# Optimization experiments

Measured on AMD Instinct MI355X. Metric: run time of the kernel, lower is better.

Reference implementation:

```python
import jax, jax.numpy as jnp
import numpy as np

# dims: d_model D, d_inner DI=2*D, d_state S, dt_rank R, conv kernel K, layers NL
D, DI, S, R, K, NL = 512, 1024, 16, 32, 4, 6
B, L = 4, 1024
EPS = 1e-5


def _ln(x, w, b):
    m = x.mean(-1, keepdims=True)
    v = ((x - m) ** 2).mean(-1, keepdims=True)
    return (x - m) * jax.lax.rsqrt(v + EPS) * w + b


def _causal_conv(x, w, b):
    # depthwise causal conv1d: x [B,L,DI], w [DI,K], left-pad K-1 (matches Conv1d(padding=K-1) then crop)
    xp = jnp.pad(x, ((0, 0), (K - 1, 0), (0, 0)))
    y = sum(xp[:, k:k + x.shape[1], :] * w[:, k] for k in range(K))
    return y + b


def _mamba(h, in_w, cw, cb, xp_w, dt_w, dt_b, A_log, Dp, out_w):
    # h: [B,L,D]
    xz = jnp.einsum('bld,ed->ble', h, in_w)        # [B,L,2*DI]
    x, z = jnp.split(xz, 2, axis=-1)
    x = jax.nn.silu(_causal_conv(x, cw, cb))       # [B,L,DI]
    dbc = jnp.einsum('bld,ed->ble', x, xp_w)       # [B,L,R+2S]
    dt_r, Bm, Cm = dbc[..., :R], dbc[..., R:R + S], dbc[..., R + S:]
    dt = jax.nn.softplus(jnp.einsum('blr,dr->bld', dt_r, dt_w) + dt_b)  # [B,L,DI]
    A = -jnp.exp(A_log)                            # [DI,S]

    def step(hst, inp):
        dt_t, B_t, C_t, x_t = inp                  # [B,DI],[B,S],[B,S],[B,DI]
        dA = jnp.exp(dt_t[..., None] * A)          # [B,DI,S]
        hst = dA * hst + (dt_t * x_t)[..., None] * B_t[:, None, :]
        y = jnp.einsum('bds,bs->bd', hst, C_t)
        return hst, y

    h0 = jnp.zeros((x.shape[0], DI, S), x.dtype)
    xs = (dt.transpose(1, 0, 2), Bm.transpose(1, 0, 2), Cm.transpose(1, 0, 2), x.transpose(1, 0, 2))
    _, ys = jax.lax.scan(step, h0, xs)
    y = ys.transpose(1, 0, 2) + x * Dp
    y = y * jax.nn.silu(z)
    return jnp.einsum('bld,ed->ble', y, out_w)     # [B,L,D]


def setup_inputs() -> dict:
    key = jax.random.key(0)
    ks = jax.random.split(key, 10)
    n = lambda k, shp, s: s * jax.random.normal(k, shp, jnp.float32)
    inp = {}
    inp['xs_pad'] = jax.random.normal(ks[0], (B, L, D), jnp.float32)
    inp['ilens'] = jax.random.randint(ks[1], (B,), 1, L + 1)
    inp['norm_w'] = jnp.ones((NL, D), jnp.float32)
    inp['norm_b'] = jnp.zeros((NL, D), jnp.float32)
    inp['in_proj_w'] = n(ks[2], (NL, 2 * DI, D), 0.02)
    inp['conv_w'] = n(ks[3], (NL, DI, K), 0.1)
    inp['conv_b'] = jnp.zeros((NL, DI), jnp.float32)
    inp['x_proj_w'] = n(ks[4], (NL, R + 2 * S, DI), 0.02)
    inp['dt_proj_w'] = n(ks[5], (NL, DI, R), 0.1)
    inp['dt_proj_b'] = n(ks[6], (NL, DI), 0.01)
    inp['A_log'] = jnp.log(jnp.broadcast_to(jnp.arange(1, S + 1, dtype=jnp.float32), (NL, DI, S)))
    inp['D_param'] = jnp.ones((NL, DI), jnp.float32)
    inp['out_proj_w'] = n(ks[7], (NL, D, DI), 0.02)
    inp['normf_w'] = jnp.ones((D,), jnp.float32)
    inp['normf_b'] = jnp.zeros((D,), jnp.float32)
    inp['after_w'] = jnp.ones((D,), jnp.float32)
    inp['after_b'] = jnp.zeros((D,), jnp.float32)
    return inp


def reference(xs_pad, ilens, norm_w, norm_b, in_proj_w, conv_w, conv_b, x_proj_w,
              dt_proj_w, dt_proj_b, A_log, D_param, out_proj_w,
              normf_w, normf_b, after_w, after_b):
    hidden = xs_pad
    residual = None
    for i in range(NL):
        residual = hidden + residual if residual is not None else hidden
        hn = _ln(residual, norm_w[i], norm_b[i])
        hidden = _mamba(hn, in_proj_w[i], conv_w[i], conv_b[i], x_proj_w[i],
                        dt_proj_w[i], dt_proj_b[i], A_log[i], D_param[i], out_proj_w[i])
    residual = hidden + residual
    out = _ln(residual, normf_w, normf_b)   # norm_f
    out = _ln(out, after_w, after_b)        # after_norm (normalize_before=True)
    olens = jnp.minimum(ilens, L)
    return out, olens
```

## Files before the change

### kernel.cpp

```cpp
#include <hip/hip_runtime.h>
#include <hip/hip_bf16.h>
#include <math.h>

#define D_   512
#define DI_  1024
#define S_   16
#define R_   32
#define KC_  4
#define NL_  6
#define B_   4
#define L_   1024
#define BL_  (B_*L_)
#define NC_  64
#define CL_  (L_/NC_)
#define BDI_ (B_*DI_)
#define LOG2E 1.44269504f
#define SKX  8
#define SKO  4

typedef __hip_bfloat16 bf16;
typedef __attribute__((ext_vector_type(8))) short bf16x8;
typedef __attribute__((ext_vector_type(4))) float f32x4;
typedef unsigned short u16;

#define QIDX(s, c, bd) (((size_t)(s) * NC_ + (c)) * BDI_ + (bd))

__device__ __forceinline__ float b2f(u16 u) {
  union { unsigned int i; float f; } x; x.i = ((unsigned int)u) << 16; return x.f;
}

__device__ __forceinline__ float softplus_f(float v) {
  float e = __expf(-fabsf(v));
  return fmaxf(v, 0.f) + __logf(1.f + e);
}

__device__ __forceinline__ void gload16(const void* g, void* l) {
  __builtin_amdgcn_global_load_lds((const __attribute__((address_space(1))) void*)g,
                                   (__attribute__((address_space(3))) void*)l, 16, 0, 0);
}

#define N1_ (NL_*2*DI_*D_)
#define N2_ (N1_ + NL_*D_*DI_)
#define N3_ (N2_ + NL_*128*DI_)
__global__ void setup_k(const float* __restrict__ in_w, const float* __restrict__ out_w,
                        const float* __restrict__ xp_w,
                        bf16* __restrict__ inw_b, bf16* __restrict__ outw_b,
                        bf16* __restrict__ xpw_b) {
  for (int i = blockIdx.x * blockDim.x + threadIdx.x; i < N3_; i += gridDim.x * blockDim.x) {
    if (i < N1_) {
      inw_b[i] = __float2bfloat16(in_w[i]);
    } else if (i < N2_) {
      int j = i - N1_;
      outw_b[j] = __float2bfloat16(out_w[j]);
    } else {
      int j = i - N2_;
      int c = j & (DI_ - 1);
      int r = (j >> 10) & 127;
      int l = j >> 17;
      float v = (r < 64) ? xp_w[((size_t)l * 64 + r) * DI_ + c] : 0.f;
      xpw_b[j] = __float2bfloat16(v);
    }
  }
}

__global__ __launch_bounds__(128) void addln_k(
    const float* __restrict__ x0, const u16* __restrict__ parts,
    float* __restrict__ resid, const float* __restrict__ w, const float* __restrict__ b,
    bf16* __restrict__ hn, int first)
{
  __shared__ float red[4];
  const int row = blockIdx.x, t = threadIdx.x;
  const int lane = t & 63, wv = t >> 6;
  float4 v;
  if (first) {
    v = *(const float4*)(x0 + (size_t)row * D_ + t * 4);
  } else {
    const size_t ps = (size_t)BL_ * D_;
    const size_t o = (size_t)row * D_ + t * 4;
    v.x = 0.f; v.y = 0.f; v.z = 0.f; v.w = 0.f;
    #pragma unroll
    for (int p = 0; p < SKO; ++p) {
      ushort4 q = *(const ushort4*)(parts + p * ps + o);
      v.x += b2f(q.x); v.y += b2f(q.y); v.z += b2f(q.z); v.w += b2f(q.w);
    }
    float4 r = *(const float4*)(resid + o);
    v.x += r.x; v.y += r.y; v.z += r.z; v.w += r.w;
  }
  *(float4*)(resid + (size_t)row * D_ + t * 4) = v;
  float s = v.x + v.y + v.z + v.w;
  float ss = v.x*v.x + v.y*v.y + v.z*v.z + v.w*v.w;
  #pragma unroll
  for (int o = 32; o > 0; o >>= 1) { s += __shfl_xor(s, o); ss += __shfl_xor(ss, o); }
  if (lane == 0) { red[wv * 2] = s; red[wv * 2 + 1] = ss; }
  __syncthreads();
  float S = red[0] + red[2], SS = red[1] + red[3];
  float m = S * (1.f / D_), var = SS * (1.f / D_) - m * m;
  float rs = rsqrtf(var + 1e-5f);
  float4 w4 = *(const float4*)(w + t * 4);
  float4 b4 = *(const float4*)(b + t * 4);
  bf16* o = hn + (size_t)row * D_ + t * 4;
  o[0] = __float2bfloat16((v.x - m) * rs * w4.x + b4.x);
  o[1] = __float2bfloat16((v.y - m) * rs * w4.y + b4.y);
  o[2] = __float2bfloat16((v.z - m) * rs * w4.z + b4.z);
  o[3] = __float2bfloat16((v.w - m) * rs * w4.w + b4.w);
}

__global__ __launch_bounds__(256) void gemm_bt(
    const bf16* __restrict__ A, int lda,
    const bf16* __restrict__ B, int ldb,
    bf16* __restrict__ Cb,
    int K, int Nact, int M, int epi)
{
  __shared__ __align__(16) bf16 As[128 * 32];
  __shared__ __align__(16) bf16 Bs[128 * 32];
  const int tid = threadIdx.x;
  const int wave = tid >> 6, lane = tid & 63;
  const int bm = blockIdx.x * 128, bn = blockIdx.y * 128;
  const int kz = blockIdx.z;
  const int Kc = K / gridDim.z;
  const int k0 = kz * Kc, k1 = k0 + Kc;
  const int wr = (wave >> 1) << 6, wc = (wave & 1) << 6;
  const int srow = lane >> 2, scg = lane & 3;
  const int rA = lane & 15, kq = (lane >> 4) << 3;
  f32x4 acc[4][4] = {};
  for (int kt = k0; kt < k1; kt += 32) {
    __syncthreads();
    #pragma unroll
    for (int p = 0; p < 2; ++p) {
      int chunk = wave * 2 + p;
      int row = (chunk << 4) + srow;
      gload16(A + (size_t)(bm + row) * lda + kt + scg * 8, &As[chunk * 512]);
      gload16(B + (size_t)(bn + row) * ldb + kt + scg * 8, &Bs[chunk * 512]);
    }
    __syncthreads();
    bf16x8 af[4], bq[4];
    #pragma unroll
    for (int m = 0; m < 4; ++m) af[m] = *(const bf16x8*)&As[(wr + m * 16 + rA) * 32 + kq];
    #pragma unroll
    for (int n = 0; n < 4; ++n) bq[n] = *(const bf16x8*)&Bs[(wc + n * 16 + rA) * 32 + kq];
    #pragma unroll
    for (int m = 0; m < 4; ++m)
      #pragma unroll
      for (int n = 0; n < 4; ++n)
        acc[m][n] = __builtin_amdgcn_mfma_f32_16x16x32_bf16(af[m], bq[n], acc[m][n], 0, 0, 0);
  }
  const int cr = (lane >> 4) << 2, cc = lane & 15;
  const size_t pbase = (epi == 1) ? (size_t)kz * M * Nact : 0;
  #pragma unroll
  for (int m = 0; m < 4; ++m)
    #pragma unroll
    for (int n = 0; n < 4; ++n) {
      int col = bn + wc + n * 16 + cc;
      if (col >= Nact) continue;
      #pragma unroll
      for (int j = 0; j < 4; ++j) {
        size_t row = (size_t)(bm + wr + m * 16 + cr + j);
        Cb[pbase + row * Nact + col] = __float2bfloat16(acc[m][n][j]);
      }
    }
}

__global__ __launch_bounds__(256) void redx_k(
    const u16* __restrict__ part, float* __restrict__ dbc)
{
  int i = blockIdx.x * 256 + threadIdx.x;
  const size_t ps = (size_t)BL_ * 64;
  float v = 0.f;
  #pragma unroll
  for (int p = 0; p < SKX; ++p) v += b2f(part[p * ps + i]);
  dbc[i] = v;
}

__global__ __launch_bounds__(256) void conv_silu_k(
    const u16* __restrict__ xz, const float* __restrict__ cw, const float* __restrict__ cb,
    bf16* __restrict__ xcb)
{
  int g = blockIdx.x * 256 + threadIdx.x;
  int dq = g & (DI_ / 8 - 1);
  int bl = g >> 7;
  int l = bl & (L_ - 1), b = bl >> 10;
  int d = dq * 8;
  float a[8], wv[8][KC_];
  #pragma unroll
  for (int e = 0; e < 8; ++e) {
    float4 w4 = *(const float4*)(cw + (d + e) * KC_);
    wv[e][0] = w4.x; wv[e][1] = w4.y; wv[e][2] = w4.z; wv[e][3] = w4.w;
    a[e] = cb[d + e];
  }
  #pragma unroll
  for (int k = 0; k < KC_; ++k) {
    int lt = l + k - 3;
    if (lt < 0) continue;
    bf16x8 xv = *(const bf16x8*)(xz + (size_t)(b * L_ + lt) * (2 * DI_) + d);
    #pragma unroll
    for (int e = 0; e < 8; ++e) a[e] += b2f((u16)xv[e]) * wv[e][k];
  }
  bf16 o8[8];
  #pragma unroll
  for (int e = 0; e < 8; ++e) {
    float v = a[e] / (1.f + __expf(-a[e]));
    o8[e] = __float2bfloat16(v);
  }
  *(bf16x8*)(xcb + (size_t)bl * DI_ + d) = *(const bf16x8*)o8;
}


__global__ __launch_bounds__(256) void scanA_k(
    const u16* __restrict__ x, const float* __restrict__ dbc,
    const float* __restrict__ dtw, const float* __restrict__ dtbias,
    const float* __restrict__ A_log, float* __restrict__ sumdt,
    bf16* __restrict__ q, bf16* __restrict__ dtb)
{
  __shared__ float BS[CL_ * 16];
  __shared__ float DTR[CL_ * 32];
  const int tid = threadIdx.x;
  int g = blockIdx.x * 256 + tid;
  int d = g & (DI_ - 1);
  int cb = g >> 10;
  int b = cb & (B_ - 1);
  int c = cb >> 2;
  {
    int step = tid >> 4, off = tid & 15;
    BS[tid] = dbc[((size_t)(b * L_ + c * CL_ + step)) * 64 + R_ + off];
    int f = tid * 2;
    int st2 = f >> 5, of2 = f & 31;
    float2 v = *(const float2*)(dbc + ((size_t)(b * L_ + c * CL_ + st2)) * 64 + of2);
    DTR[f] = v.x; DTR[f + 1] = v.y;
  }
  float wv[R_];
  #pragma unroll
  for (int r = 0; r < R_; r += 4) {
    float4 w4 = *(const float4*)(dtw + (size_t)d * R_ + r);
    wv[r] = w4.x; wv[r + 1] = w4.y; wv[r + 2] = w4.z; wv[r + 3] = w4.w;
  }
  const float bias = dtbias[d];
  const float An2b = -expf(A_log[(size_t)d * S_]) * LOG2E;
  bool fast = true;
  #pragma unroll
  for (int s = 1; s < S_; ++s) {
    float a = -expf(A_log[(size_t)d * S_ + s]) * LOG2E;
    fast = fast && (fabsf(a - (float)(s + 1) * An2b) <= 1e-5f * fabsf(a));
  }
  __syncthreads();
  float h[S_] = {};
  float sdt = 0.f;
  const size_t base = ((size_t)b * L_ + c * CL_) * DI_ + d;
  float cx = b2f(x[base]);
  float dtv;
  {
    float v = bias;
    #pragma unroll
    for (int r = 0; r < R_; r += 4) {
      float4 dv = *(const float4*)&DTR[r];
      v += dv.x * wv[r] + dv.y * wv[r + 1] + dv.z * wv[r + 2] + dv.w * wv[r + 3];
    }
    dtv = softplus_f(v);
  }
  for (int i = 0; i < CL_; ++i) {
    const int ip = (i + 1 < CL_) ? i + 1 : i;
    float nx = b2f(x[base + (size_t)ip * DI_]);
    float vn = bias;
    #pragma unroll
    for (int r = 0; r < R_; r += 4) {
      float4 dv = *(const float4*)&DTR[ip * 32 + r];
      vn += dv.x * wv[r] + dv.y * wv[r + 1] + dv.z * wv[r + 2] + dv.w * wv[r + 3];
    }
    dtb[base + (size_t)i * DI_] = __float2bfloat16(dtv);
    sdt += dtv;
    float u = dtv * cx;
    float Bv[S_];
    *(float4*)&Bv[0]  = *(const float4*)&BS[i * 16 + 0];
    *(float4*)&Bv[4]  = *(const float4*)&BS[i * 16 + 4];
    *(float4*)&Bv[8]  = *(const float4*)&BS[i * 16 + 8];
    *(float4*)&Bv[12] = *(const float4*)&BS[i * 16 + 12];
    float da[S_];
    if (fast) {
      float E1 = exp2f(dtv * An2b);
      float E2 = E1 * E1;
      float E4 = E2 * E2;
      da[0] = E1; da[1] = E2; da[2] = E2 * E1; da[3] = E4;
      #pragma unroll
      for (int s = 4; s < S_; ++s) da[s] = da[s - 4] * E4;
    } else {
      #pragma unroll
      for (int s = 0; s < S_; ++s)
        da[s] = exp2f(dtv * (-expf(A_log[(size_t)d * S_ + s]) * LOG2E));
    }
    #pragma unroll
    for (int s = 0; s < S_; ++s) h[s] = da[s] * h[s] + u * Bv[s];
    dtv = softplus_f(vn);
    cx = nx;
  }
  int bd = b * DI_ + d;
  sumdt[(size_t)c * BDI_ + bd] = sdt;
  #pragma unroll
  for (int s = 0; s < S_; ++s) q[QIDX(s, c, bd)] = __float2bfloat16(h[s]);
}

__global__ __launch_bounds__(256) void scanB_k(
    const float* __restrict__ sumdt, const u16* __restrict__ q,
    const float* __restrict__ A_log, bf16* __restrict__ hi)
{
  int g = blockIdx.x * 256 + threadIdx.x;
  int s = g >> 12;
  int bd = g & (BDI_ - 1);
  int d = bd & (DI_ - 1);
  float An2 = -expf(A_log[(size_t)d * S_ + s]) * LOG2E;
  float h = 0.f;
  float sd = sumdt[bd];
  float qq = b2f(q[(size_t)s * NC_ * BDI_ + bd]);
  for (int c = 0; c < NC_; ++c) {
    float sdn = sd, qn = qq;
    if (c + 1 < NC_) {
      sdn = sumdt[(size_t)(c + 1) * BDI_ + bd];
      qn  = b2f(q[QIDX(s, c + 1, bd)]);
    }
    hi[QIDX(s, c, bd)] = __float2bfloat16(h);
    h = exp2f(An2 * sd) * h + qq;
    sd = sdn; qq = qn;
  }
}

__global__ __launch_bounds__(256) void scanC_k(
    const u16* __restrict__ dt, const u16* __restrict__ x, const float* __restrict__ dbc,
    const float* __restrict__ A_log, const float* __restrict__ Dp, const u16* __restrict__ xz,
    const u16* __restrict__ hi, bf16* __restrict__ y)
{
  __shared__ float BCS[CL_ * 32];
  const int tid = threadIdx.x;
  int g = blockIdx.x * 256 + tid;
  int d = g & (DI_ - 1);
  int cb = g >> 10;
  int b = cb & (B_ - 1);
  int c = cb >> 2;
  {
    int f = tid * 2;
    int step = f >> 5, off = f & 31;
    float2 v = *(const float2*)(dbc + ((size_t)(b * L_ + c * CL_ + step)) * 64 + R_ + off);
    BCS[f] = v.x; BCS[f + 1] = v.y;
  }
  const float An2b = -expf(A_log[(size_t)d * S_]) * LOG2E;
  bool fast = true;
  #pragma unroll
  for (int s = 1; s < S_; ++s) {
    float a = -expf(A_log[(size_t)d * S_ + s]) * LOG2E;
    fast = fast && (fabsf(a - (float)(s + 1) * An2b) <= 1e-5f * fabsf(a));
  }
  int bd = b * DI_ + d;
  float h[S_];
  #pragma unroll
  for (int s = 0; s < S_; ++s) h[s] = b2f(hi[QIDX(s, c, bd)]);
  __syncthreads();
  float dpv = Dp[d];
  const size_t rid0 = (size_t)b * L_ + c * CL_;
  const size_t base = rid0 * DI_ + d;
  float cdt = b2f(dt[base]), cx = b2f(x[base]);
  float cz = b2f(xz[rid0 * (2 * DI_) + DI_ + d]);
  float Ecur = exp2f(cdt * An2b);
  for (int i = 0; i < CL_; ++i) {
    const int ip = (i + 1 < CL_) ? i + 1 : i;
    float ndt = b2f(dt[base + (size_t)ip * DI_]);
    float nx  = b2f(x[base + (size_t)ip * DI_]);
    float nz  = b2f(xz[(rid0 + ip) * (2 * DI_) + DI_ + d]);
    float Enext = exp2f(ndt * An2b);
    float u = cdt * cx;
    float Bv[S_], Cv[S_];
    *(float4*)&Bv[0]  = *(const float4*)&BCS[i * 32 + 0];
    *(float4*)&Bv[4]  = *(const float4*)&BCS[i * 32 + 4];
    *(float4*)&Bv[8]  = *(const float4*)&BCS[i * 32 + 8];
    *(float4*)&Bv[12] = *(const float4*)&BCS[i * 32 + 12];
    *(float4*)&Cv[0]  = *(const float4*)&BCS[i * 32 + 16];
    *(float4*)&Cv[4]  = *(const float4*)&BCS[i * 32 + 20];
    *(float4*)&Cv[8]  = *(const float4*)&BCS[i * 32 + 24];
    *(float4*)&Cv[12] = *(const float4*)&BCS[i * 32 + 28];
    float da[S_];
    if (fast) {
      float E1 = Ecur;
      float E2 = E1 * E1;
      float E4 = E2 * E2;
      da[0] = E1; da[1] = E2; da[2] = E2 * E1; da[3] = E4;
      #pragma unroll
      for (int s = 4; s < S_; ++s) da[s] = da[s - 4] * E4;
    } else {
      #pragma unroll
      for (int s = 0; s < S_; ++s)
        da[s] = exp2f(cdt * (-expf(A_log[(size_t)d * S_ + s]) * LOG2E));
    }
    float acc = 0.f;
    #pragma unroll
    for (int s = 0; s < S_; ++s) {
      h[s] = da[s] * h[s] + u * Bv[s];
      acc += h[s] * Cv[s];
    }
    acc += cx * dpv;
    acc *= cz / (1.f + __expf(-cz));
    y[(rid0 + i) * DI_ + d] = __float2bfloat16(acc);
    cdt = ndt; cx = nx; cz = nz; Ecur = Enext;
  }
}

__global__ __launch_bounds__(128) void final_k(
    const u16* __restrict__ parts, const float* __restrict__ res,
    const float* __restrict__ fw, const float* __restrict__ fb,
    const float* __restrict__ aw, const float* __restrict__ ab,
    const int* __restrict__ ilens, float* __restrict__ out, int outN)
{
  __shared__ float red[4];
  const int row = blockIdx.x, t = threadIdx.x;
  const int lane = t & 63, wv = t >> 6;
  const size_t ps = (size_t)BL_ * D_;
  const size_t o0 = (size_t)row * D_ + t * 4;
  float4 v; v.x = 0.f; v.y = 0.f; v.z = 0.f; v.w = 0.f;
  #pragma unroll
  for (int p = 0; p < SKO; ++p) {
    ushort4 q = *(const ushort4*)(parts + p * ps + o0);
    v.x += b2f(q.x); v.y += b2f(q.y); v.z += b2f(q.z); v.w += b2f(q.w);
  }
  float4 r = *(const float4*)(res + o0);
  v.x += r.x; v.y += r.y; v.z += r.z; v.w += r.w;
  float s = v.x + v.y + v.z + v.w;
  float ss = v.x*v.x + v.y*v.y + v.z*v.z + v.w*v.w;
  #pragma unroll
  for (int o = 32; o > 0; o >>= 1) { s += __shfl_xor(s, o); ss += __shfl_xor(ss, o); }
  if (lane == 0) { red[wv * 2] = s; red[wv * 2 + 1] = ss; }
  __syncthreads();
  float S = red[0] + red[2], SS = red[1] + red[3];
  float m = S * (1.f / D_), var = SS * (1.f / D_) - m * m;
  float rs = rsqrtf(var + 1e-5f);
  float4 w4 = *(const float4*)(fw + t * 4);
  float4 b4 = *(const float4*)(fb + t * 4);
  float4 x1;
  x1.x = (v.x - m) * rs * w4.x + b4.x;
  x1.y = (v.y - m) * rs * w4.y + b4.y;
  x1.z = (v.z - m) * rs * w4.z + b4.z;
  x1.w = (v.w - m) * rs * w4.w + b4.w;
  __syncthreads();
  float s2 = x1.x + x1.y + x1.z + x1.w;
  float ss2 = x1.x*x1.x + x1.y*x1.y + x1.z*x1.z + x1.w*x1.w;
  #pragma unroll
  for (int o = 32; o > 0; o >>= 1) { s2 += __shfl_xor(s2, o); ss2 += __shfl_xor(ss2, o); }
  if (lane == 0) { red[wv * 2] = s2; red[wv * 2 + 1] = ss2; }
  __syncthreads();
  float S2 = red[0] + red[2], SS2 = red[1] + red[3];
  float m2 = S2 * (1.f / D_), var2 = SS2 * (1.f / D_) - m2 * m2;
  float rs2 = rsqrtf(var2 + 1e-5f);
  float4 aw4 = *(const float4*)(aw + t * 4);
  float4 ab4 = *(const float4*)(ab + t * 4);
  float4 o;
  o.x = (x1.x - m2) * rs2 * aw4.x + ab4.x;
  o.y = (x1.y - m2) * rs2 * aw4.y + ab4.y;
  o.z = (x1.z - m2) * rs2 * aw4.z + ab4.z;
  o.w = (x1.w - m2) * rs2 * aw4.w + ab4.w;
  *(float4*)(out + (size_t)row * D_ + t * 4) = o;
  if (row == 0 && t < B_) {
    int q = ilens[t];
    out[outN + t] = (float)(q < L_ ? q : L_);
  }
}

extern "C" void kernel_launch(void* const* d_in, const int* in_sizes, int n_in,
                              void* d_out, int out_size, void* d_ws, size_t ws_size,
                              hipStream_t stream) {
  const float* xs     = (const float*)d_in[0];
  const int*   ilens  = (const int*)d_in[1];
  const float* norm_w = (const float*)d_in[2];
  const float* norm_b = (const float*)d_in[3];
  const float* in_w   = (const float*)d_in[4];
  const float* conv_w = (const float*)d_in[5];
  const float* conv_b = (const float*)d_in[6];
  const float* xp_w   = (const float*)d_in[7];
  const float* dt_w   = (const float*)d_in[8];
  const float* dt_b   = (const float*)d_in[9];
  const float* A_log  = (const float*)d_in[10];
  const float* Dp     = (const float*)d_in[11];
  const float* out_w  = (const float*)d_in[12];
  const float* nfw    = (const float*)d_in[13];
  const float* nfb    = (const float*)d_in[14];
  const float* afw    = (const float*)d_in[15];
  const float* afb    = (const float*)d_in[16];
  float* out = (float*)d_out;

  char* ws = (char*)d_ws;
  size_t off = 0;
  auto alloc = [&](size_t bytes) -> char* {
    char* p = ws + off;
    off += (bytes + 255) & ~(size_t)255;
    return p;
  };
  bf16*  inw_b  = (bf16*)alloc((size_t)NL_ * 2 * DI_ * D_ * 2);
  bf16*  outw_b = (bf16*)alloc((size_t)NL_ * D_ * DI_ * 2);
  bf16*  xpw_b  = (bf16*)alloc((size_t)NL_ * 128 * DI_ * 2);
  float* resid  = (float*)alloc((size_t)BL_ * D_ * 4);
  bf16*  hn_b   = (bf16*)alloc((size_t)BL_ * D_ * 2);
  bf16*  xzb    = (bf16*)alloc((size_t)BL_ * 2 * DI_ * 2);
  bf16*  xcb    = (bf16*)alloc((size_t)BL_ * DI_ * 2);
  bf16*  xpart  = (bf16*)alloc((size_t)SKX * BL_ * 64 * 2);
  float* dbc    = (float*)alloc((size_t)BL_ * 64 * 4);
  bf16*  dtb    = (bf16*)alloc((size_t)BL_ * DI_ * 2);
  float* sdt    = (float*)alloc((size_t)NC_ * BDI_ * 4);
  bf16*  qb     = (bf16*)alloc((size_t)S_ * NC_ * BDI_ * 2);
  bf16*  hini   = (bf16*)alloc((size_t)S_ * NC_ * BDI_ * 2);
  bf16*  yb     = (bf16*)alloc((size_t)BL_ * DI_ * 2);
  bf16*  opart  = (bf16*)alloc((size_t)SKO * BL_ * D_ * 2);
  if (off > ws_size) return;

  setup_k<<<4096, 256, 0, stream>>>(in_w, out_w, xp_w, inw_b, outw_b, xpw_b);

  for (int i = 0; i < NL_; ++i) {
    addln_k<<<BL_, 128, 0, stream>>>(xs, (const u16*)opart, resid,
                                     norm_w + i * D_, norm_b + i * D_, hn_b, i == 0);
    dim3 g1(32, 16, 1);
    gemm_bt<<<g1, 256, 0, stream>>>(hn_b, D_, inw_b + (size_t)i * 2 * DI_ * D_, D_,
                                    xzb, D_, 2 * DI_, BL_, 3);
    conv_silu_k<<<(BL_ * DI_ / 8) / 256, 256, 0, stream>>>(
        (const u16*)xzb, conv_w + i * DI_ * KC_, conv_b + i * DI_, xcb);
    dim3 g2(32, 1, SKX);
    gemm_bt<<<g2, 256, 0, stream>>>(xcb, DI_, xpw_b + (size_t)i * 128 * DI_, DI_,
                                    xpart, DI_, 64, BL_, 1);
    redx_k<<<(BL_ * 64) / 256, 256, 0, stream>>>((const u16*)xpart, dbc);
    scanA_k<<<(NC_ * B_ * DI_) / 256, 256, 0, stream>>>(
        (const u16*)xcb, dbc, dt_w + (size_t)i * DI_ * R_, dt_b + i * DI_,
        A_log + (size_t)i * DI_ * S_, sdt, qb, dtb);
    scanB_k<<<(B_ * DI_ * S_) / 256, 256, 0, stream>>>(
        sdt, (const u16*)qb, A_log + (size_t)i * DI_ * S_, hini);
    scanC_k<<<(NC_ * B_ * DI_) / 256, 256, 0, stream>>>(
        (const u16*)dtb, (const u16*)xcb, dbc, A_log + (size_t)i * DI_ * S_, Dp + i * DI_,
        (const u16*)xzb, (const u16*)hini, yb);
    dim3 g4(32, 4, SKO);
    gemm_bt<<<g4, 256, 0, stream>>>(yb, DI_, outw_b + (size_t)i * D_ * DI_, DI_,
                                    opart, DI_, D_, BL_, 1);
  }
  final_k<<<BL_, 128, 0, stream>>>((const u16*)opart, resid, nfw, nfb, afw, afb, ilens, out,
                                   out_size - B_);
}
```

Before: 728.4 us.

## Fuse x_proj split-K reduction into scan kernels and halve chunk length

Removes the separate redx_k kernel and its fp32 dbc buffer. The scanA and scanC kernels now sum the eight bf16 split-K partials directly while filling shared memory. The scan chunk count is doubled, which halves chunk length and gives more blocks to the chunked scan passes, and the inner per-step loops are fully unrolled. In exchange, each block redoes the partial reduction for its rows, the serial inter-chunk pass in scanB gets twice as long, and the q and hini buffers double in size.

```diff
diff --git a/kernel.cpp b/kernel.cpp
--- a/kernel.cpp
+++ b/kernel.cpp
@@ -11,7 +11,7 @@
 #define B_   4
 #define L_   1024
 #define BL_  (B_*L_)
-#define NC_  64
+#define NC_  128
 #define CL_  (L_/NC_)
 #define BDI_ (B_*DI_)
 #define LOG2E 1.44269504f
@@ -160,17 +160,6 @@
     }
 }
 
-__global__ __launch_bounds__(256) void redx_k(
-    const u16* __restrict__ part, float* __restrict__ dbc)
-{
-  int i = blockIdx.x * 256 + threadIdx.x;
-  const size_t ps = (size_t)BL_ * 64;
-  float v = 0.f;
-  #pragma unroll
-  for (int p = 0; p < SKX; ++p) v += b2f(part[p * ps + i]);
-  dbc[i] = v;
-}
-
 __global__ __launch_bounds__(256) void conv_silu_k(
     const u16* __restrict__ xz, const float* __restrict__ cw, const float* __restrict__ cb,
     bf16* __restrict__ xcb)
@@ -206,13 +195,12 @@
 
 
 __global__ __launch_bounds__(256) void scanA_k(
-    const u16* __restrict__ x, const float* __restrict__ dbc,
+    const u16* __restrict__ x, const u16* __restrict__ xpart,
     const float* __restrict__ dtw, const float* __restrict__ dtbias,
     const float* __restrict__ A_log, float* __restrict__ sumdt,
     bf16* __restrict__ q, bf16* __restrict__ dtb)
 {
-  __shared__ float BS[CL_ * 16];
-  __shared__ float DTR[CL_ * 32];
+  __shared__ float SM[CL_ * 48];
   const int tid = threadIdx.x;
   int g = blockIdx.x * 256 + tid;
   int d = g & (DI_ - 1);
@@ -220,12 +208,15 @@
   int b = cb & (B_ - 1);
   int c = cb >> 2;
   {
-    int step = tid >> 4, off = tid & 15;
-    BS[tid] = dbc[((size_t)(b * L_ + c * CL_ + step)) * 64 + R_ + off];
-    int f = tid * 2;
-    int st2 = f >> 5, of2 = f & 31;
-    float2 v = *(const float2*)(dbc + ((size_t)(b * L_ + c * CL_ + st2)) * 64 + of2);
-    DTR[f] = v.x; DTR[f + 1] = v.y;
+    const size_t ps = (size_t)BL_ * 64;
+    for (int idx = tid; idx < CL_ * 48; idx += 256) {
+      int row = idx / 48, col = idx - row * 48;
+      size_t rb = ((size_t)(b * L_ + c * CL_ + row)) * 64 + col;
+      float v = 0.f;
+      #pragma unroll
+      for (int p = 0; p < SKX; ++p) v += b2f(xpart[p * ps + rb]);
+      SM[idx] = v;
+    }
   }
   float wv[R_];
   #pragma unroll
@@ -251,28 +242,29 @@
     float v = bias;
     #pragma unroll
     for (int r = 0; r < R_; r += 4) {
-      float4 dv = *(const float4*)&DTR[r];
+      float4 dv = *(const float4*)&SM[r];
       v += dv.x * wv[r] + dv.y * wv[r + 1] + dv.z * wv[r + 2] + dv.w * wv[r + 3];
     }
     dtv = softplus_f(v);
   }
+  #pragma unroll
   for (int i = 0; i < CL_; ++i) {
     const int ip = (i + 1 < CL_) ? i + 1 : i;
     float nx = b2f(x[base + (size_t)ip * DI_]);
     float vn = bias;
     #pragma unroll
     for (int r = 0; r < R_; r += 4) {
-      float4 dv = *(const float4*)&DTR[ip * 32 + r];
+      float4 dv = *(const float4*)&SM[ip * 48 + r];
       vn += dv.x * wv[r] + dv.y * wv[r + 1] + dv.z * wv[r + 2] + dv.w * wv[r + 3];
     }
     dtb[base + (size_t)i * DI_] = __float2bfloat16(dtv);
     sdt += dtv;
     float u = dtv * cx;
     float Bv[S_];
-    *(float4*)&Bv[0]  = *(const float4*)&BS[i * 16 + 0];
-    *(float4*)&Bv[4]  = *(const float4*)&BS[i * 16 + 4];
-    *(float4*)&Bv[8]  = *(const float4*)&BS[i * 16 + 8];
-    *(float4*)&Bv[12] = *(const float4*)&BS[i * 16 + 12];
+    *(float4*)&Bv[0]  = *(const float4*)&SM[i * 48 + 32];
+    *(float4*)&Bv[4]  = *(const float4*)&SM[i * 48 + 36];
+    *(float4*)&Bv[8]  = *(const float4*)&SM[i * 48 + 40];
+    *(float4*)&Bv[12] = *(const float4*)&SM[i * 48 + 44];
     float da[S_];
     if (fast) {
       float E1 = exp2f(dtv * An2b);
@@ -322,11 +314,11 @@
 }
 
 __global__ __launch_bounds__(256) void scanC_k(
-    const u16* __restrict__ dt, const u16* __restrict__ x, const float* __restrict__ dbc,
+    const u16* __restrict__ dt, const u16* __restrict__ x, const u16* __restrict__ xpart,
     const float* __restrict__ A_log, const float* __restrict__ Dp, const u16* __restrict__ xz,
     const u16* __restrict__ hi, bf16* __restrict__ y)
 {
-  __shared__ float BCS[CL_ * 32];
+  __shared__ float SM[CL_ * 32];
   const int tid = threadIdx.x;
   int g = blockIdx.x * 256 + tid;
   int d = g & (DI_ - 1);
@@ -334,10 +326,13 @@
   int b = cb & (B_ - 1);
   int c = cb >> 2;
   {
-    int f = tid * 2;
-    int step = f >> 5, off = f & 31;
-    float2 v = *(const float2*)(dbc + ((size_t)(b * L_ + c * CL_ + step)) * 64 + R_ + off);
-    BCS[f] = v.x; BCS[f + 1] = v.y;
+    const size_t ps = (size_t)BL_ * 64;
+    int row = tid >> 5, col = tid & 31;
+    size_t rb = ((size_t)(b * L_ + c * CL_ + row)) * 64 + 32 + col;
+    float v = 0.f;
+    #pragma unroll
+    for (int p = 0; p < SKX; ++p) v += b2f(xpart[p * ps + rb]);
+    SM[tid] = v;
   }
   const float An2b = -expf(A_log[(size_t)d * S_]) * LOG2E;
   bool fast = true;
@@ -357,6 +352,7 @@
   float cdt = b2f(dt[base]), cx = b2f(x[base]);
   float cz = b2f(xz[rid0 * (2 * DI_) + DI_ + d]);
   float Ecur = exp2f(cdt * An2b);
+  #pragma unroll
   for (int i = 0; i < CL_; ++i) {
     const int ip = (i + 1 < CL_) ? i + 1 : i;
     float ndt = b2f(dt[base + (size_t)ip * DI_]);
@@ -365,14 +361,14 @@
     float Enext = exp2f(ndt * An2b);
     float u = cdt * cx;
     float Bv[S_], Cv[S_];
-    *(float4*)&Bv[0]  = *(const float4*)&BCS[i * 32 + 0];
-    *(float4*)&Bv[4]  = *(const float4*)&BCS[i * 32 + 4];
-    *(float4*)&Bv[8]  = *(const float4*)&BCS[i * 32 + 8];
-    *(float4*)&Bv[12] = *(const float4*)&BCS[i * 32 + 12];
-    *(float4*)&Cv[0]  = *(const float4*)&BCS[i * 32 + 16];
-    *(float4*)&Cv[4]  = *(const float4*)&BCS[i * 32 + 20];
-    *(float4*)&Cv[8]  = *(const float4*)&BCS[i * 32 + 24];
-    *(float4*)&Cv[12] = *(const float4*)&BCS[i * 32 + 28];
+    *(float4*)&Bv[0]  = *(const float4*)&SM[i * 32 + 0];
+    *(float4*)&Bv[4]  = *(const float4*)&SM[i * 32 + 4];
+    *(float4*)&Bv[8]  = *(const float4*)&SM[i * 32 + 8];
+    *(float4*)&Bv[12] = *(const float4*)&SM[i * 32 + 12];
+    *(float4*)&Cv[0]  = *(const float4*)&SM[i * 32 + 16];
+    *(float4*)&Cv[4]  = *(const float4*)&SM[i * 32 + 20];
+    *(float4*)&Cv[8]  = *(const float4*)&SM[i * 32 + 24];
+    *(float4*)&Cv[12] = *(const float4*)&SM[i * 32 + 28];
     float da[S_];
     if (fast) {
       float E1 = Ecur;
@@ -495,7 +491,6 @@
   bf16*  xzb    = (bf16*)alloc((size_t)BL_ * 2 * DI_ * 2);
   bf16*  xcb    = (bf16*)alloc((size_t)BL_ * DI_ * 2);
   bf16*  xpart  = (bf16*)alloc((size_t)SKX * BL_ * 64 * 2);
-  float* dbc    = (float*)alloc((size_t)BL_ * 64 * 4);
   bf16*  dtb    = (bf16*)alloc((size_t)BL_ * DI_ * 2);
   float* sdt    = (float*)alloc((size_t)NC_ * BDI_ * 4);
   bf16*  qb     = (bf16*)alloc((size_t)S_ * NC_ * BDI_ * 2);
@@ -517,14 +512,14 @@
     dim3 g2(32, 1, SKX);
     gemm_bt<<<g2, 256, 0, stream>>>(xcb, DI_, xpw_b + (size_t)i * 128 * DI_, DI_,
                                     xpart, DI_, 64, BL_, 1);
-    redx_k<<<(BL_ * 64) / 256, 256, 0, stream>>>((const u16*)xpart, dbc);
     scanA_k<<<(NC_ * B_ * DI_) / 256, 256, 0, stream>>>(
-        (const u16*)xcb, dbc, dt_w + (size_t)i * DI_ * R_, dt_b + i * DI_,
+        (const u16*)xcb, (const u16*)xpart, dt_w + (size_t)i * DI_ * R_, dt_b + i * DI_,
         A_log + (size_t)i * DI_ * S_, sdt, qb, dtb);
     scanB_k<<<(B_ * DI_ * S_) / 256, 256, 0, stream>>>(
         sdt, (const u16*)qb, A_log + (size_t)i * DI_ * S_, hini);
     scanC_k<<<(NC_ * B_ * DI_) / 256, 256, 0, stream>>>(
-        (const u16*)dtb, (const u16*)xcb, dbc, A_log + (size_t)i * DI_ * S_, Dp + i * DI_,
+        (const u16*)dtb, (const u16*)xcb, (const u16*)xpart,
+        A_log + (size_t)i * DI_ * S_, Dp + i * DI_,
         (const u16*)xzb, (const u16*)hini, yb);
     dim3 g4(32, 4, SKO);
     gemm_bt<<<g4, 256, 0, stream>>>(yb, DI_, outw_b + (size_t)i * D_ * DI_, DI_,
```

Result: slower. 997.1 us (+36.9%).
